# Performance work log

Hardware: AMD Instinct MI355X
Metric: run time of the kernel (lower is better)

The kernel has to match this reference:

```python
import jax, jax.numpy as jnp
import numpy as np

B = 16384      # batch of Monte Carlo paths
N = 100        # time steps
DIM_W = 3
DT = 0.01
SQRT_DT = DT ** 0.5
SIGMA0 = 0.5   # constant diffusion coefficient (concrete sigma = SIGMA0 * ones(B,1,DIM_W))


def _mlp(x, W1, b1, W2, b2, W3, b3):
    h = jax.nn.relu(x @ W1 + b1)
    h = jax.nn.relu(h @ W2 + b2)
    return h @ W3 + b3


def setup_inputs() -> dict:
    key = jax.random.key(0)
    ks = jax.random.split(key, 8)
    s = 0.1  # modest weight scale for numerical sanity
    return {
        'y0': jnp.ones((1,), jnp.float32),
        'Y0': jnp.zeros((1, 1), jnp.float32),
        'zW1': s * jax.random.normal(ks[0], (2, 64), jnp.float32),
        'zb1': jnp.zeros((64,), jnp.float32),
        'zW2': s * jax.random.normal(ks[1], (64, 64), jnp.float32),
        'zb2': jnp.zeros((64,), jnp.float32),
        'zW3': s * jax.random.normal(ks[2], (64, 3), jnp.float32),
        'zb3': jnp.zeros((3,), jnp.float32),
        'qW1': s * jax.random.normal(ks[3], (2, 64), jnp.float32),
        'qb1': jnp.zeros((64,), jnp.float32),
        'qW2': s * jax.random.normal(ks[4], (64, 64), jnp.float32),
        'qb2': jnp.zeros((64,), jnp.float32),
        'qW3': s * jax.random.normal(ks[5], (64, 1), jnp.float32),
        'qb3': jnp.zeros((1,), jnp.float32),
        'dW': jax.random.normal(ks[6], (N, B, DIM_W), jnp.float32),
        'dZ': jax.random.normal(ks[7], (N, B, DIM_W), jnp.float32),
    }


def reference(y0, Y0, zW1, zb1, zW2, zb2, zW3, zb3,
              qW1, qb1, qW2, qb2, qW3, qb3, dW, dZ):
    y = jnp.broadcast_to(y0.reshape(1, 1), (B, 1))          # (B,1) state
    Y = jnp.broadcast_to(Y0, (B, 1))                         # (B,1) value process
    t = jnp.zeros((B, 1), jnp.float32)

    def step(carry, noise):
        y, Y, t, loss_acc = carry
        dWi, dZi = noise
        inp = jnp.concatenate([t, y], axis=1)                # (B,2)
        z = _mlp(inp, zW1, zb1, zW2, zb2, zW3, zb3)          # (B,3)
        q = _mlp(inp, qW1, qb1, qW2, qb2, qW3, qb3)          # (B,1)
        f = 0.5 * q * q                                      # generator (B,1)
        dw = dWi * SQRT_DT
        dz = dZi * SQRT_DT
        # sigma = SIGMA0 * ones(B,1,DIM_W); bmm(sigma, dw) = SIGMA0 * sum_j dw_j
        diffusion = SIGMA0 * jnp.sum(dw, axis=1, keepdims=True)
        y_new = y + q * DT + diffusion                       # mu = q
        Y_next = Y - f * DT + jnp.sum(z * dw, axis=1, keepdims=True)
        residual = Y_next - (Y - f * DT + jnp.sum(z * dz, axis=1, keepdims=True))
        loss_acc = loss_acc + jnp.mean(residual * residual)
        return (y_new, Y_next, t + DT, loss_acc), None

    (y, Y, t, total_residual_loss), _ = jax.lax.scan(
        step, (y, Y, t, jnp.float32(0.0)), (dW, dZ))
    terminal = y * y                                         # terminal_cost(y)
    terminal_loss = jnp.mean((Y - terminal) ** 2)
    return terminal_loss + total_residual_loss
```

## Files before the change

### kernel.cpp

```cpp
#include <hip/hip_runtime.h>
#include <hip/hip_bf16.h>

#define BATCH   16384
#define NSTEPS  100
#define DT_     0.01f
#define SQRTDT  0.1f
#define SIGMA0_ 0.5f

typedef _Float16  f16x2  __attribute__((ext_vector_type(2)));
typedef _Float16  f16x4  __attribute__((ext_vector_type(4)));
typedef _Float16  f16x8  __attribute__((ext_vector_type(8)));
typedef __fp16    h16x2  __attribute__((ext_vector_type(2)));
typedef float     f32x4  __attribute__((ext_vector_type(4)));

typedef const __attribute__((address_space(1))) void* gas_ptr;
typedef __attribute__((address_space(3))) void*       las_ptr;

__global__ void zero_out_kernel(float* out) { if (threadIdx.x == 0) out[0] = 0.0f; }

static __device__ __forceinline__ f16x4 pk4(const f32x4& d) {
    union { h16x2 h[2]; f16x4 v; } c;
    c.h[0] = __builtin_amdgcn_cvt_pkrtz(d[0], d[1]);
    c.h[1] = __builtin_amdgcn_cvt_pkrtz(d[2], d[3]);
    return c.v;
}

__launch_bounds__(256, 2)
__global__ void deepbsde_kernel(
    const float* __restrict__ y0,  const float* __restrict__ Y0,
    const float* __restrict__ zW1, const float* __restrict__ zb1,
    const float* __restrict__ zW2, const float* __restrict__ zb2,
    const float* __restrict__ zW3, const float* __restrict__ zb3,
    const float* __restrict__ qW1, const float* __restrict__ qb1,
    const float* __restrict__ qW2, const float* __restrict__ qb2,
    const float* __restrict__ qW3, const float* __restrict__ qb3,
    const float* __restrict__ dW,  const float* __restrict__ dZ,
    float* __restrict__ out)
{
    __shared__ __align__(16) char zring[2][8][384];
    __shared__ __align__(16) char qring[2][8][192];
    __shared__ __align__(16) _Float16 tbl[NSTEPS * 128];
    __shared__ float yring[2][NSTEPS + 1][16];
    __shared__ float ffin[2][16];
    __shared__ int   flags[2][2];

    const int tid  = threadIdx.x;
    const int lane = tid & 63;
    const int w    = tid >> 6;
    const int g    = w >> 1;
    const int flip = (((int)blockIdx.x >> 3) ^ ((int)blockIdx.x >> 8)) & 1;
    const bool isQ = ((w & 1) ^ flip) != 0;
    const int ln15 = lane & 15, q4 = lane >> 4;
    const int gw   = (blockIdx.x << 1) + g;
    const int pbase = gw << 4;

    if (tid < 4) ((int*)flags)[tid] = 0;

    auto fillz = [&](int i) {
        if (lane < 24) {
            const char* gp = (lane < 12)
                ? (const char*)dW + ((size_t)i * BATCH + pbase) * 12 + (size_t)lane * 16
                : (const char*)dZ + ((size_t)i * BATCH + pbase) * 12 + (size_t)(lane - 12) * 16;
            __builtin_amdgcn_global_load_lds((gas_ptr)gp, (las_ptr)&zring[g][i & 7][0],
                                             16, 0, 0);
        }
    };
    auto fillq = [&](int i) {
        if (lane < 12) {
            const char* gp = (const char*)dW + ((size_t)i * BATCH + pbase) * 12 + (size_t)lane * 16;
            __builtin_amdgcn_global_load_lds((gas_ptr)gp, (las_ptr)&qring[g][i & 7][0],
                                             16, 0, 0);
        }
    };
    if (!isQ) { fillz(0); fillz(1); fillz(2); fillz(3); }
    else      { fillq(0); fillq(1); fillq(2); fillq(3); }

    {
        float tt = 0.0f;
        for (int i = 0; i < NSTEPS; ++i) {
            int r = (tid - (i << 6)) & 255;
            if (r < 64) {
                int q4e = r >> 4, mlp_ = (r >> 3) & 1, m = r & 7;
                const float* Wp = mlp_ ? qW1 : zW1;
                const float* bp = mlp_ ? qb1 : zb1;
                int i0 = 2*m, i1 = 2*m + 1;
                int k0 = 32*(i0 >> 3) + 8*q4e + (i0 & 7);
                int k1 = 32*(i1 >> 3) + 8*q4e + (i1 & 7);
                _Float16 th = (_Float16)tt;
                f16x2 A = {(_Float16)Wp[k0], (_Float16)Wp[k1]};
                f16x2 C = {(_Float16)bp[k0], (_Float16)bp[k1]};
                f16x2 tv = {th, th};
                f16x2 v = A*tv + C;
                int idx = (i*4 + q4e)*16 + mlp_*8 + m;
                *(f16x2*)&tbl[idx << 1] = v;
            }
            tt += DT_;
        }
    }

    const float* W1p = isQ ? qW1 : zW1;
    const float* W2p = isQ ? qW2 : zW2;
    const float* b2p = isQ ? qb2 : zb2;

    f16x2 B1[8];
#pragma unroll
    for (int m = 0; m < 8; ++m) {
        int i0 = 2*m, i1 = 2*m + 1;
        int k0 = 32*(i0 >> 3) + 8*q4 + (i0 & 7);
        int k1 = 32*(i1 >> 3) + 8*q4 + (i1 & 7);
        B1[m] = (f16x2){(_Float16)W1p[64 + k0], (_Float16)W1p[64 + k1]};
    }

    f16x8 Af[4][2];
#pragma unroll
    for (int tN = 0; tN < 4; ++tN)
#pragma unroll
        for (int f = 0; f < 2; ++f)
#pragma unroll
            for (int j = 0; j < 8; ++j) {
                int k = 32*f + 8*q4 + j, n = 16*tN + ln15;
                Af[tN][f][j] = (_Float16)W2p[k*64 + n];
            }

    f32x4 b2v[4];
#pragma unroll
    for (int tN = 0; tN < 4; ++tN)
#pragma unroll
        for (int r = 0; r < 4; ++r)
            b2v[tN][r] = b2p[16*tN + 4*q4 + r];

    const int c3 = ln15 & 3;
    f16x8 A3[2];
#pragma unroll
    for (int fl = 0; fl < 2; ++fl)
#pragma unroll
        for (int j = 0; j < 8; ++j) {
            int tN = 2*fl + (j >> 2);
            int n  = 16*tN + 4*q4 + (j & 3);
            float wv = isQ ? ((c3 == 3) ? qW3[n]                 : 0.0f)
                           : ((c3 < 3)  ? SQRTDT * zW3[n*3 + c3] : 0.0f);
            A3[fl][j] = (_Float16)wv;
        }

    const f32x4 C3b = isQ ? (f32x4){0.0f, 0.0f, 0.0f, qb3[0]}
                          : (f32x4){SQRTDT*zb3[0], SQRTDT*zb3[1], SQRTDT*zb3[2], 0.0f};

    const float CSIG = SIGMA0_ * SQRTDT;
    const float NHDT = -0.5f * DT_;
    const float y0v = y0[0], Y0v = Y0[0];

    const f16x2 zero2h = {(_Float16)0.0f, (_Float16)0.0f};
    const f16x4 zero4h = {(_Float16)0.0f, (_Float16)0.0f, (_Float16)0.0f, (_Float16)0.0f};

    if (isQ && q4 == 0) *(volatile float*)&yring[g][0][ln15] = y0v;

    __syncthreads();

    if (!isQ) {
        float Ysum = 0.0f, acc = 0.0f;
        float ya, yb, yc, yd;

        auto ybatch = [&](int base) {
            volatile int* qf = &flags[g][0];
            while (*qf < base + 4) { }
            ya = *(volatile float*)&yring[g][base + 0][ln15];
            yb = *(volatile float*)&yring[g][base + 1][ln15];
            yc = *(volatile float*)&yring[g][base + 2][ln15];
            yd = *(volatile float*)&yring[g][base + 3][ln15];
        };

        auto zpair = [&](int iA, float yA, int iB, float yB) {
            const float* sA = (const float*)&zring[g][iA & 7][0];
            const float* sB = (const float*)&zring[g][iB & 7][0];
            float aw0 = sA[ln15*3+0], aw1 = sA[ln15*3+1], aw2 = sA[ln15*3+2];
            float az0 = sA[48+ln15*3+0], az1 = sA[48+ln15*3+1], az2 = sA[48+ln15*3+2];
            float bw0 = sB[ln15*3+0], bw1 = sB[ln15*3+1], bw2 = sB[ln15*3+2];
            float bz0_ = sB[48+ln15*3+0], bz1_ = sB[48+ln15*3+1], bz2_ = sB[48+ln15*3+2];

            const f16x8* tpA = (const f16x8*)(tbl + (iA*4 + q4)*32);
            const f16x8* tpB = (const f16x8*)(tbl + (iB*4 + q4)*32);
            union U8 { f16x8 v; f16x2 h[4]; };
            U8 TA0; TA0.v = tpA[0]; U8 TA1; TA1.v = tpA[1];
            U8 TB0; TB0.v = tpB[0]; U8 TB1; TB1.v = tpB[1];

            _Float16 yhA = (_Float16)yA, yhB = (_Float16)yB;
            const f16x2 yvA = {yhA, yhA}, yvB = {yhB, yhB};
            union { f16x2 h[4]; f16x8 v; } a0, a1, b0, b1;
#pragma unroll
            for (int m = 0; m < 4; ++m) {
                a0.h[m] = __builtin_elementwise_max((f16x2)(B1[m]*yvA   + TA0.h[m]), zero2h);
                b0.h[m] = __builtin_elementwise_max((f16x2)(B1[m]*yvB   + TB0.h[m]), zero2h);
                a1.h[m] = __builtin_elementwise_max((f16x2)(B1[m+4]*yvA + TA1.h[m]), zero2h);
                b1.h[m] = __builtin_elementwise_max((f16x2)(B1[m+4]*yvB + TB1.h[m]), zero2h);
            }

            union { f16x4 q[4]; f16x8 o[2]; } BA, BB;
#pragma unroll
            for (int tN = 0; tN < 4; ++tN) {
                f32x4 dA = b2v[tN];
                f32x4 dB = b2v[tN];
                dA = __builtin_amdgcn_mfma_f32_16x16x32_f16(Af[tN][0], a0.v, dA, 0, 0, 0);
                dB = __builtin_amdgcn_mfma_f32_16x16x32_f16(Af[tN][0], b0.v, dB, 0, 0, 0);
                dA = __builtin_amdgcn_mfma_f32_16x16x32_f16(Af[tN][1], a1.v, dA, 0, 0, 0);
                dB = __builtin_amdgcn_mfma_f32_16x16x32_f16(Af[tN][1], b1.v, dB, 0, 0, 0);
                BA.q[tN] = __builtin_elementwise_max(pk4(dA), zero4h);
                BB.q[tN] = __builtin_elementwise_max(pk4(dB), zero4h);
            }

            f32x4 PA = C3b, PB = C3b;
            PA = __builtin_amdgcn_mfma_f32_16x16x32_f16(A3[0], BA.o[0], PA, 0, 0, 0);
            PB = __builtin_amdgcn_mfma_f32_16x16x32_f16(A3[0], BB.o[0], PB, 0, 0, 0);
            PA = __builtin_amdgcn_mfma_f32_16x16x32_f16(A3[1], BA.o[1], PA, 0, 0, 0);
            PB = __builtin_amdgcn_mfma_f32_16x16x32_f16(A3[1], BB.o[1], PB, 0, 0, 0);

            float zdwA = fmaf(PA[2], aw2, fmaf(PA[1], aw1, PA[0]*aw0));
            float zdzA = fmaf(PA[2], az2, fmaf(PA[1], az1, PA[0]*az0));
            Ysum += zdwA;
            float rA = zdwA - zdzA;
            acc = fmaf(rA, rA, acc);
            float zdwB = fmaf(PB[2], bw2, fmaf(PB[1], bw1, PB[0]*bw0));
            float zdzB = fmaf(PB[2], bz2_, fmaf(PB[1], bz1_, PB[0]*bz0_));
            Ysum += zdwB;
            float rB = zdwB - zdzB;
            acc = fmaf(rB, rB, acc);
        };

#pragma unroll 1
        for (int b = 0; b < 24; ++b) {
            int i = 4*b;
            ybatch(i);
            __builtin_amdgcn_s_waitcnt(0x0F72);
            fillz(i + 4); fillz(i + 5);
            zpair(i,     ya, i + 1, yb);
            __builtin_amdgcn_s_waitcnt(0x0F72);
            fillz(i + 6); fillz(i + 7);
            zpair(i + 2, yc, i + 3, yd);
        }
        ybatch(96);
        __builtin_amdgcn_s_waitcnt(0x0F72);
        zpair(96, ya, 97, yb);
        __builtin_amdgcn_s_waitcnt(0x0F70);
        zpair(98, yc, 99, yd);

        {
            volatile int* qf = &flags[g][0];
            while (*qf < NSTEPS + 1) { }
        }
        float Fq = *(volatile float*)&ffin[g][ln15];
        float yT = *(volatile float*)&yring[g][NSTEPS][ln15];
        float Yvf = Y0v + Fq + Ysum;
        float dterm = Yvf - yT*yT;
        acc = fmaf(dterm, dterm, acc);

        float val = (q4 == 0) ? acc : 0.0f;
#pragma unroll
        for (int off = 1; off < 64; off <<= 1) val += __shfl_xor(val, off);
        if (lane == 0) atomicAdd(out, val * (1.0f / BATCH));
    } else {
        __builtin_amdgcn_s_setprio(1);
        float y = y0v, Facc = 0.0f;
        f16x8 c0, c1, d0, d1;
        { const f16x8* tp = (const f16x8*)(tbl + q4*32); c0 = tp[2]; c1 = tp[3]; }

        auto qbody = [&](int j, f16x8& t0, f16x8& t1, f16x8& u0, f16x8& u1) {
            const float* sl = (const float*)&qring[g][j & 7][0];
            float nw0 = sl[ln15*3 + 0], nw1 = sl[ln15*3 + 1], nw2 = sl[ln15*3 + 2];
            int jp = j + 1; jp = (jp > NSTEPS - 1) ? NSTEPS - 1 : jp;
            { const f16x8* tp = (const f16x8*)(tbl + (jp*4 + q4)*32); u0 = tp[2]; u1 = tp[3]; }

            _Float16 yh = (_Float16)y;
            const f16x2 yv = {yh, yh};
            union U8 { f16x8 v; f16x2 h[4]; };
            U8 T0; T0.v = t0; U8 T1; T1.v = t1;
            union { f16x2 h[4]; f16x8 v; } b0, b1;
#pragma unroll
            for (int m = 0; m < 4; ++m) {
                b0.h[m] = __builtin_elementwise_max((f16x2)(B1[m]*yv   + T0.h[m]), zero2h);
                b1.h[m] = __builtin_elementwise_max((f16x2)(B1[m+4]*yv + T1.h[m]), zero2h);
            }
            union { f16x4 q[4]; f16x8 o[2]; } Bh;
#pragma unroll
            for (int tN = 0; tN < 4; ++tN) {
                f32x4 d = b2v[tN];
                d = __builtin_amdgcn_mfma_f32_16x16x32_f16(Af[tN][0], b0.v, d, 0, 0, 0);
                d = __builtin_amdgcn_mfma_f32_16x16x32_f16(Af[tN][1], b1.v, d, 0, 0, 0);
                Bh.q[tN] = __builtin_elementwise_max(pk4(d), zero4h);
            }
            f32x4 Pv = C3b;
            Pv = __builtin_amdgcn_mfma_f32_16x16x32_f16(A3[0], Bh.o[0], Pv, 0, 0, 0);
            Pv = __builtin_amdgcn_mfma_f32_16x16x32_f16(A3[1], Bh.o[1], Pv, 0, 0, 0);

            float qv = Pv[3];
            float snw = (nw0 + nw1) + nw2;
            Facc = fmaf(NHDT*qv, qv, Facc);
            y = fmaf(CSIG, snw, fmaf(qv, DT_, y));
            if (q4 == 0) *(volatile float*)&yring[g][j + 1][ln15] = y;
        };

#pragma unroll 1
        for (int jb = 0; jb < 24; ++jb) {
            int j = 4*jb;
            __builtin_amdgcn_s_waitcnt(0x0F73); fillq(j + 4);
            qbody(j,     c0, c1, d0, d1);
            __builtin_amdgcn_s_waitcnt(0x0F73); fillq(j + 5);
            qbody(j + 1, d0, d1, c0, c1);
            __builtin_amdgcn_s_waitcnt(0x0F73); fillq(j + 6);
            qbody(j + 2, c0, c1, d0, d1);
            __builtin_amdgcn_s_waitcnt(0x0F73); fillq(j + 7);
            qbody(j + 3, d0, d1, c0, c1);
            __builtin_amdgcn_s_waitcnt(0xC07F);
            if (lane == 0) *(volatile int*)&flags[g][0] = j + 4;
        }
        __builtin_amdgcn_s_waitcnt(0x0F73);
        qbody(96, c0, c1, d0, d1);
        __builtin_amdgcn_s_waitcnt(0x0F72);
        qbody(97, d0, d1, c0, c1);
        __builtin_amdgcn_s_waitcnt(0x0F71);
        qbody(98, c0, c1, d0, d1);
        __builtin_amdgcn_s_waitcnt(0x0F70);
        qbody(99, d0, d1, c0, c1);
        __builtin_amdgcn_s_waitcnt(0xC07F);
        if (lane == 0) *(volatile int*)&flags[g][0] = NSTEPS;

        if (q4 == 0) *(volatile float*)&ffin[g][ln15] = Facc;
        __builtin_amdgcn_s_waitcnt(0xC07F);
        if (lane == 0) *(volatile int*)&flags[g][0] = NSTEPS + 1;
    }
}

extern "C" void kernel_launch(void* const* d_in, const int* in_sizes, int n_in,
                              void* d_out, int out_size, void* d_ws, size_t ws_size,
                              hipStream_t stream)
{
    zero_out_kernel<<<1, 64, 0, stream>>>((float*)d_out);
    deepbsde_kernel<<<512, 256, 0, stream>>>(
        (const float*)d_in[0],  (const float*)d_in[1],
        (const float*)d_in[2],  (const float*)d_in[3],
        (const float*)d_in[4],  (const float*)d_in[5],
        (const float*)d_in[6],  (const float*)d_in[7],
        (const float*)d_in[8],  (const float*)d_in[9],
        (const float*)d_in[10], (const float*)d_in[11],
        (const float*)d_in[12], (const float*)d_in[13],
        (const float*)d_in[14], (const float*)d_in[15],
        (float*)d_out);
}
```

Before: 155.8 us.

## Replace LDS ring prefetch of noise with register-resident 8-deep global loads

Drops the global_load_lds ring buffers for dW/dZ. Each lane now loads its own three noise floats straight into registers, keeping eight steps in flight and unrolling the loops by 8 with register rotation. This removes LDS staging, the explicit vmcnt waits and the LDS reads, which were costs on the serial critical path. In exchange it raises register pressure, issues more small uncoalesced 4-byte global loads, and relies on compiler-inserted waits.

Result: slower. 159.3 us (+2.3%).

```diff
diff --git a/kernel.cpp b/kernel.cpp
--- a/kernel.cpp
+++ b/kernel.cpp
@@ -12,9 +12,6 @@
 typedef _Float16  f16x8  __attribute__((ext_vector_type(8)));
 typedef __fp16    h16x2  __attribute__((ext_vector_type(2)));
 typedef float     f32x4  __attribute__((ext_vector_type(4)));
-
-typedef const __attribute__((address_space(1))) void* gas_ptr;
-typedef __attribute__((address_space(3))) void*       las_ptr;
 
 __global__ void zero_out_kernel(float* out) { if (threadIdx.x == 0) out[0] = 0.0f; }
 
@@ -24,6 +21,8 @@
     c.h[1] = __builtin_amdgcn_cvt_pkrtz(d[2], d[3]);
     return c.v;
 }
+
+struct N3 { float a, b, c; };
 
 __launch_bounds__(256, 2)
 __global__ void deepbsde_kernel(
@@ -37,8 +36,6 @@
     const float* __restrict__ dW,  const float* __restrict__ dZ,
     float* __restrict__ out)
 {
-    __shared__ __align__(16) char zring[2][8][384];
-    __shared__ __align__(16) char qring[2][8][192];
     __shared__ __align__(16) _Float16 tbl[NSTEPS * 128];
     __shared__ float yring[2][NSTEPS + 1][16];
     __shared__ float ffin[2][16];
@@ -55,25 +52,6 @@
     const int pbase = gw << 4;
 
     if (tid < 4) ((int*)flags)[tid] = 0;
-
-    auto fillz = [&](int i) {
-        if (lane < 24) {
-            const char* gp = (lane < 12)
-                ? (const char*)dW + ((size_t)i * BATCH + pbase) * 12 + (size_t)lane * 16
-                : (const char*)dZ + ((size_t)i * BATCH + pbase) * 12 + (size_t)(lane - 12) * 16;
-            __builtin_amdgcn_global_load_lds((gas_ptr)gp, (las_ptr)&zring[g][i & 7][0],
-                                             16, 0, 0);
-        }
-    };
-    auto fillq = [&](int i) {
-        if (lane < 12) {
-            const char* gp = (const char*)dW + ((size_t)i * BATCH + pbase) * 12 + (size_t)lane * 16;
-            __builtin_amdgcn_global_load_lds((gas_ptr)gp, (las_ptr)&qring[g][i & 7][0],
-                                             16, 0, 0);
-        }
-    };
-    if (!isQ) { fillz(0); fillz(1); fillz(2); fillz(3); }
-    else      { fillq(0); fillq(1); fillq(2); fillq(3); }
 
     {
         float tt = 0.0f;
@@ -156,6 +134,17 @@
 
     __syncthreads();
 
+    auto loadW = [&](int i, N3& d) {
+        int ic = (i < NSTEPS) ? i : NSTEPS - 1;
+        const float* p = dW + ((size_t)ic * BATCH + pbase + ln15) * 3;
+        d.a = p[0]; d.b = p[1]; d.c = p[2];
+    };
+    auto loadZ = [&](int i, N3& d) {
+        int ic = (i < NSTEPS) ? i : NSTEPS - 1;
+        const float* p = dZ + ((size_t)ic * BATCH + pbase + ln15) * 3;
+        d.a = p[0]; d.b = p[1]; d.c = p[2];
+    };
+
     if (!isQ) {
         float Ysum = 0.0f, acc = 0.0f;
         float ya, yb, yc, yd;
@@ -169,14 +158,8 @@
             yd = *(volatile float*)&yring[g][base + 3][ln15];
         };
 
-        auto zpair = [&](int iA, float yA, int iB, float yB) {
-            const float* sA = (const float*)&zring[g][iA & 7][0];
-            const float* sB = (const float*)&zring[g][iB & 7][0];
-            float aw0 = sA[ln15*3+0], aw1 = sA[ln15*3+1], aw2 = sA[ln15*3+2];
-            float az0 = sA[48+ln15*3+0], az1 = sA[48+ln15*3+1], az2 = sA[48+ln15*3+2];
-            float bw0 = sB[ln15*3+0], bw1 = sB[ln15*3+1], bw2 = sB[ln15*3+2];
-            float bz0_ = sB[48+ln15*3+0], bz1_ = sB[48+ln15*3+1], bz2_ = sB[48+ln15*3+2];
-
+        auto zpair = [&](int iA, float yA, int iB, float yB,
+                         const N3& wA, const N3& zA, const N3& wB, const N3& zB) {
             const f16x8* tpA = (const f16x8*)(tbl + (iA*4 + q4)*32);
             const f16x8* tpB = (const f16x8*)(tbl + (iB*4 + q4)*32);
             union U8 { f16x8 v; f16x2 h[4]; };
@@ -213,34 +196,45 @@
             PA = __builtin_amdgcn_mfma_f32_16x16x32_f16(A3[1], BA.o[1], PA, 0, 0, 0);
             PB = __builtin_amdgcn_mfma_f32_16x16x32_f16(A3[1], BB.o[1], PB, 0, 0, 0);
 
-            float zdwA = fmaf(PA[2], aw2, fmaf(PA[1], aw1, PA[0]*aw0));
-            float zdzA = fmaf(PA[2], az2, fmaf(PA[1], az1, PA[0]*az0));
+            float zdwA = fmaf(PA[2], wA.c, fmaf(PA[1], wA.b, PA[0]*wA.a));
+            float zdzA = fmaf(PA[2], zA.c, fmaf(PA[1], zA.b, PA[0]*zA.a));
             Ysum += zdwA;
             float rA = zdwA - zdzA;
             acc = fmaf(rA, rA, acc);
-            float zdwB = fmaf(PB[2], bw2, fmaf(PB[1], bw1, PB[0]*bw0));
-            float zdzB = fmaf(PB[2], bz2_, fmaf(PB[1], bz1_, PB[0]*bz0_));
+            float zdwB = fmaf(PB[2], wB.c, fmaf(PB[1], wB.b, PB[0]*wB.a));
+            float zdzB = fmaf(PB[2], zB.c, fmaf(PB[1], zB.b, PB[0]*zB.a));
             Ysum += zdwB;
             float rB = zdwB - zdzB;
             acc = fmaf(rB, rB, acc);
         };
 
+        N3 w0,w1,w2,w3,w4,w5,w6,w7, z0,z1,z2,z3,z4,z5,z6,z7;
+        loadW(0,w0); loadZ(0,z0); loadW(1,w1); loadZ(1,z1);
+        loadW(2,w2); loadZ(2,z2); loadW(3,w3); loadZ(3,z3);
+        loadW(4,w4); loadZ(4,z4); loadW(5,w5); loadZ(5,z5);
+        loadW(6,w6); loadZ(6,z6); loadW(7,w7); loadZ(7,z7);
+
 #pragma unroll 1
-        for (int b = 0; b < 24; ++b) {
-            int i = 4*b;
+        for (int k = 0; k < 12; ++k) {
+            int i = 8*k;
             ybatch(i);
-            __builtin_amdgcn_s_waitcnt(0x0F72);
-            fillz(i + 4); fillz(i + 5);
-            zpair(i,     ya, i + 1, yb);
-            __builtin_amdgcn_s_waitcnt(0x0F72);
-            fillz(i + 6); fillz(i + 7);
-            zpair(i + 2, yc, i + 3, yd);
+            zpair(i,     ya, i + 1, yb, w0, z0, w1, z1);
+            loadW(i + 8,  w0); loadZ(i + 8,  z0);
+            loadW(i + 9,  w1); loadZ(i + 9,  z1);
+            zpair(i + 2, yc, i + 3, yd, w2, z2, w3, z3);
+            loadW(i + 10, w2); loadZ(i + 10, z2);
+            loadW(i + 11, w3); loadZ(i + 11, z3);
+            ybatch(i + 4);
+            zpair(i + 4, ya, i + 5, yb, w4, z4, w5, z5);
+            loadW(i + 12, w4); loadZ(i + 12, z4);
+            loadW(i + 13, w5); loadZ(i + 13, z5);
+            zpair(i + 6, yc, i + 7, yd, w6, z6, w7, z7);
+            loadW(i + 14, w6); loadZ(i + 14, z6);
+            loadW(i + 15, w7); loadZ(i + 15, z7);
         }
         ybatch(96);
-        __builtin_amdgcn_s_waitcnt(0x0F72);
-        zpair(96, ya, 97, yb);
-        __builtin_amdgcn_s_waitcnt(0x0F70);
-        zpair(98, yc, 99, yd);
+        zpair(96, ya, 97, yb, w0, z0, w1, z1);
+        zpair(98, yc, 99, yd, w2, z2, w3, z3);
 
         {
             volatile int* qf = &flags[g][0];
@@ -262,9 +256,7 @@
         f16x8 c0, c1, d0, d1;
         { const f16x8* tp = (const f16x8*)(tbl + q4*32); c0 = tp[2]; c1 = tp[3]; }
 
-        auto qbody = [&](int j, f16x8& t0, f16x8& t1, f16x8& u0, f16x8& u1) {
-            const float* sl = (const float*)&qring[g][j & 7][0];
-            float nw0 = sl[ln15*3 + 0], nw1 = sl[ln15*3 + 1], nw2 = sl[ln15*3 + 2];
+        auto qbody = [&](int j, const N3& nw, f16x8& t0, f16x8& t1, f16x8& u0, f16x8& u1) {
             int jp = j + 1; jp = (jp > NSTEPS - 1) ? NSTEPS - 1 : jp;
             { const f16x8* tp = (const f16x8*)(tbl + (jp*4 + q4)*32); u0 = tp[2]; u1 = tp[3]; }
 
@@ -291,34 +283,36 @@
             Pv = __builtin_amdgcn_mfma_f32_16x16x32_f16(A3[1], Bh.o[1], Pv, 0, 0, 0);
 
             float qv = Pv[3];
-            float snw = (nw0 + nw1) + nw2;
+            float snw = (nw.a + nw.b) + nw.c;
             Facc = fmaf(NHDT*qv, qv, Facc);
             y = fmaf(CSIG, snw, fmaf(qv, DT_, y));
             if (q4 == 0) *(volatile float*)&yring[g][j + 1][ln15] = y;
         };
 
+        N3 n0,n1,n2,n3,n4,n5,n6,n7;
+        loadW(0,n0); loadW(1,n1); loadW(2,n2); loadW(3,n3);
+        loadW(4,n4); loadW(5,n5); loadW(6,n6); loadW(7,n7);
+
 #pragma unroll 1
-        for (int jb = 0; jb < 24; ++jb) {
-            int j = 4*jb;
-            __builtin_amdgcn_s_waitcnt(0x0F73); fillq(j + 4);
-            qbody(j,     c0, c1, d0, d1);
-            __builtin_amdgcn_s_waitcnt(0x0F73); fillq(j + 5);
-            qbody(j + 1, d0, d1, c0, c1);
-            __builtin_amdgcn_s_waitcnt(0x0F73); fillq(j + 6);
-            qbody(j + 2, c0, c1, d0, d1);
-            __builtin_amdgcn_s_waitcnt(0x0F73); fillq(j + 7);
-            qbody(j + 3, d0, d1, c0, c1);
+        for (int k = 0; k < 12; ++k) {
+            int j = 8*k;
+            qbody(j,     n0, c0, c1, d0, d1);  loadW(j + 8,  n0);
+            qbody(j + 1, n1, d0, d1, c0, c1);  loadW(j + 9,  n1);
+            qbody(j + 2, n2, c0, c1, d0, d1);  loadW(j + 10, n2);
+            qbody(j + 3, n3, d0, d1, c0, c1);  loadW(j + 11, n3);
             __builtin_amdgcn_s_waitcnt(0xC07F);
             if (lane == 0) *(volatile int*)&flags[g][0] = j + 4;
-        }
-        __builtin_amdgcn_s_waitcnt(0x0F73);
-        qbody(96, c0, c1, d0, d1);
-        __builtin_amdgcn_s_waitcnt(0x0F72);
-        qbody(97, d0, d1, c0, c1);
-        __builtin_amdgcn_s_waitcnt(0x0F71);
-        qbody(98, c0, c1, d0, d1);
-        __builtin_amdgcn_s_waitcnt(0x0F70);
-        qbody(99, d0, d1, c0, c1);
+            qbody(j + 4, n4, c0, c1, d0, d1);  loadW(j + 12, n4);
+            qbody(j + 5, n5, d0, d1, c0, c1);  loadW(j + 13, n5);
+            qbody(j + 6, n6, c0, c1, d0, d1);  loadW(j + 14, n6);
+            qbody(j + 7, n7, d0, d1, c0, c1);  loadW(j + 15, n7);
+            __builtin_amdgcn_s_waitcnt(0xC07F);
+            if (lane == 0) *(volatile int*)&flags[g][0] = j + 8;
+        }
+        qbody(96, n0, c0, c1, d0, d1);
+        qbody(97, n1, d0, d1, c0, c1);
+        qbody(98, n2, c0, c1, d0, d1);
+        qbody(99, n3, d0, d1, c0, c1);
         __builtin_amdgcn_s_waitcnt(0xC07F);
         if (lane == 0) *(volatile int*)&flags[g][0] = NSTEPS;
 
```
